# Optimization experiments

Measured on AMD Instinct MI355X. Metric: run time of the kernel, lower is better.

The kernel has to match this reference:

```python
import math
import jax, jax.numpy as jnp
import numpy as np

B, T, C, H = 4, 1024, 1024, 16


def setup_inputs() -> dict:
    key = jax.random.key(0)
    k1, k2, k3 = jax.random.split(key, 3)
    scale = 0.02
    return {
        "x": jax.random.normal(k1, (B, T, C), dtype=jnp.float32),
        "w_attn": jax.random.normal(k2, (C, 3 * C), dtype=jnp.float32) * scale,
        "b_attn": jnp.zeros((3 * C,), dtype=jnp.float32),
        "w_proj": jax.random.normal(k3, (C, C), dtype=jnp.float32) * scale,
        "b_proj": jnp.zeros((C,), dtype=jnp.float32),
    }


def reference(x, w_attn, b_attn, w_proj, b_proj):
    b, t, c = x.shape
    h = H
    d = c // h
    qkv = x @ w_attn + b_attn                      # [b, t, 3c]
    q, k, v = jnp.split(qkv, 3, axis=-1)
    # [b, h, t, d]
    q = q.reshape(b, t, h, d).transpose(0, 2, 1, 3)
    k = k.reshape(b, t, h, d).transpose(0, 2, 1, 3)
    v = v.reshape(b, t, h, d).transpose(0, 2, 1, 3)
    att = jnp.einsum("bhqd,bhkd->bhqk", q, k) * (1.0 / math.sqrt(d))
    causal = jnp.tril(jnp.ones((t, t), dtype=bool))
    att = jnp.where(causal[None, None], att, -jnp.inf)
    att = jax.nn.softmax(att, axis=-1)
    # dropout is identity in eval mode
    y = jnp.einsum("bhqk,bhkd->bhqd", att, v)      # [b, h, t, d]
    y = y.transpose(0, 2, 1, 3).reshape(b, t, c)
    return y @ w_proj + b_proj
```

## Files before the change

### kernel.cpp

```cpp
#include <hip/hip_runtime.h>

typedef __bf16 bf16;
typedef float f32x4 __attribute__((ext_vector_type(4)));
typedef bf16 bf16x4 __attribute__((ext_vector_type(4)));
typedef bf16 bf16x8 __attribute__((ext_vector_type(8)));

#define MFMA16(a, b, c) __builtin_amdgcn_mfma_f32_16x16x32_bf16((a), (b), (c), 0, 0, 0)

__device__ __forceinline__ f32x4 zero4() {
    f32x4 z; z[0] = 0.f; z[1] = 0.f; z[2] = 0.f; z[3] = 0.f; return z;
}
__device__ __forceinline__ void gl_lds16(const bf16* g, bf16* l) {
    __builtin_amdgcn_global_load_lds(
        (const __attribute__((address_space(1))) void*)g,
        (__attribute__((address_space(3))) void*)l, 16, 0, 0);
}

__global__ __launch_bounds__(256) void conv_k(const float* __restrict__ src,
                                              bf16* __restrict__ dst, int n)
{
    const int i = (blockIdx.x * 256 + threadIdx.x) * 8;
    if (i >= n) return;
    const float4 a = *(const float4*)(src + i);
    const float4 b = *(const float4*)(src + i + 4);
    bf16x8 o;
    o[0] = (bf16)a.x; o[1] = (bf16)a.y; o[2] = (bf16)a.z; o[3] = (bf16)a.w;
    o[4] = (bf16)b.x; o[5] = (bf16)b.y; o[6] = (bf16)b.z; o[7] = (bf16)b.w;
    *(bf16x8*)(dst + i) = o;
}

__global__ __launch_bounds__(256) void transp_k(const float* __restrict__ src,
                                                bf16* __restrict__ dst, int K, int N)
{
    __shared__ bf16 Ls[64][72];
    const int tid = threadIdx.x;
    const int k0 = blockIdx.y << 6;
    const int n0 = blockIdx.x << 6;
    #pragma unroll
    for (int it = 0; it < 4; ++it) {
        const int lin = (it << 10) + (tid << 2);
        const int r = lin >> 6, c = lin & 63;
        const float4 v = *(const float4*)(src + (size_t)(k0 + r) * N + n0 + c);
        bf16x4 o; o[0] = (bf16)v.x; o[1] = (bf16)v.y; o[2] = (bf16)v.z; o[3] = (bf16)v.w;
        *(bf16x4*)&Ls[r][c] = o;
    }
    __syncthreads();
    #pragma unroll
    for (int it = 0; it < 2; ++it) {
        const int lin = (it << 11) + (tid << 3);
        const int nn = lin >> 6, kk = lin & 63;
        bf16x8 o;
        #pragma unroll
        for (int j = 0; j < 8; ++j) o[j] = Ls[kk + j][nn];
        *(bf16x8*)(dst + (size_t)(n0 + nn) * K + k0 + kk) = o;
    }
}

template <int MODE, int BN>
__global__ __launch_bounds__(256)
void gemm_bt(const bf16* __restrict__ A, const bf16* __restrict__ Bt,
             const float* __restrict__ bias,
             bf16* __restrict__ qw, bf16* __restrict__ kw, bf16* __restrict__ vw,
             float* __restrict__ outf, int M, int N, int K)
{
    constexpr int BK = 32;
    constexpr int MF = (BN == 128) ? 4 : 2;
    constexpr int NF = 4;
    constexpr int AE = 128 * BK;
    constexpr int BE = BN * BK;

    __shared__ __align__(16) bf16 smem[2 * AE + 2 * BE];
    bf16* const As0 = smem;
    bf16* const As1 = smem + AE;
    bf16* const Bs0 = smem + 2 * AE;
    bf16* const Bs1 = smem + 2 * AE + BE;

    const int tid  = threadIdx.x;
    const int lane = tid & 63;
    const int wid  = tid >> 6;
    const int l16  = lane & 15;
    const int g    = lane >> 4;
    const int wrb  = (BN == 128) ? ((wid >> 1) << 6) : (wid << 5);
    const int wcb  = (BN == 128) ? ((wid & 1) << 6) : 0;
    const int m0   = blockIdx.y << 7;
    const int n0   = blockIdx.x * BN;

    const int srow = lane >> 2;
    const int schk = lane & 3;
    const int rA0 = (wid << 5) + srow;
    const int rA1 = rA0 + 16;
    const int rB0 = wid * (BN / 4) + srow;
    const int rB1 = rB0 + 16;
    const bf16* pa0 = A  + (size_t)(m0 + rA0) * K + ((schk ^ ((rA0 >> 1) & 3)) << 3);
    const bf16* pa1 = A  + (size_t)(m0 + rA1) * K + ((schk ^ ((rA1 >> 1) & 3)) << 3);
    const bf16* pb0 = Bt + (size_t)(n0 + rB0) * K + ((schk ^ ((rB0 >> 1) & 3)) << 3);
    const bf16* pb1 = Bt + (size_t)(n0 + rB1) * K + ((schk ^ ((rB1 >> 1) & 3)) << 3);
    const int dA0 = (wid << 5) * BK, dA1 = dA0 + 16 * BK;
    const int dB0 = (wid * (BN / 4)) * BK, dB1 = dB0 + 16 * BK;

    int offA[MF], offB[NF];
    #pragma unroll
    for (int mf = 0; mf < MF; ++mf) {
        const int r = wrb + (mf << 4) + l16;
        offA[mf] = r * BK + ((g ^ ((r >> 1) & 3)) << 3);
    }
    #pragma unroll
    for (int nf = 0; nf < NF; ++nf) {
        const int r = wcb + (nf << 4) + l16;
        offB[nf] = r * BK + ((g ^ ((r >> 1) & 3)) << 3);
    }

    f32x4 acc[MF][NF];
    #pragma unroll
    for (int i = 0; i < MF; ++i)
        #pragma unroll
        for (int j = 0; j < NF; ++j) acc[i][j] = zero4();

    const int nk = K >> 5;
    gl_lds16(pa0, As0 + dA0); gl_lds16(pa1, As0 + dA1);
    gl_lds16(pb0, Bs0 + dB0);
    if (BN == 128) gl_lds16(pb1, Bs0 + dB1);
    pa0 += BK; pa1 += BK; pb0 += BK; pb1 += BK;
    __syncthreads();

    for (int kt = 0; kt < nk; ++kt) {
        const bool odd = kt & 1;
        if (kt + 1 < nk) {
            bf16* an = odd ? As0 : As1;
            bf16* bn = odd ? Bs0 : Bs1;
            gl_lds16(pa0, an + dA0); gl_lds16(pa1, an + dA1);
            gl_lds16(pb0, bn + dB0);
            if (BN == 128) gl_lds16(pb1, bn + dB1);
            pa0 += BK; pa1 += BK; pb0 += BK; pb1 += BK;
        }
        const bf16* ac = odd ? As1 : As0;
        const bf16* bc = odd ? Bs1 : Bs0;
        bf16x8 af[MF], bfr[NF];
        #pragma unroll
        for (int mf = 0; mf < MF; ++mf) af[mf] = *(const bf16x8*)&ac[offA[mf]];
        #pragma unroll
        for (int nf = 0; nf < NF; ++nf) bfr[nf] = *(const bf16x8*)&bc[offB[nf]];
        #pragma unroll
        for (int mf = 0; mf < MF; ++mf)
            #pragma unroll
            for (int nf = 0; nf < NF; ++nf)
                acc[mf][nf] = MFMA16(af[mf], bfr[nf], acc[mf][nf]);
        __syncthreads();
    }

    if (MODE == 0) {
        bf16* const Es = smem;
        const int bq  = m0 >> 10;
        const int tb  = m0 & 1023;
        const int hh0 = (n0 & 1023) >> 6;
        const bool isV = (n0 >= 2048);
        if (isV) {
            #pragma unroll
            for (int mf = 0; mf < MF; ++mf)
                #pragma unroll
                for (int nf = 0; nf < NF; ++nf) {
                    const int nn = wcb + (nf << 4) + l16;
                    const float bs = bias[n0 + nn];
                    bf16x4 p;
                    #pragma unroll
                    for (int j = 0; j < 4; ++j) p[j] = (bf16)(acc[mf][nf][j] + bs);
                    const int m = wrb + (mf << 4) + (g << 2);
                    const int pp = ((m >> 5) << 5) + (((m >> 2) & 3) << 3) + (((m >> 4) & 1) << 2);
                    *(bf16x4*)&Es[nn * 128 + pp] = p;
                }
        } else {
            #pragma unroll
            for (int mf = 0; mf < MF; ++mf)
                #pragma unroll
                for (int nf = 0; nf < NF; ++nf) {
                    const int nn = wcb + (nf << 4) + l16;
                    const float bs = bias[n0 + nn];
                    #pragma unroll
                    for (int j = 0; j < 4; ++j) {
                        const int mm = wrb + (mf << 4) + (g << 2) + j;
                        Es[mm * 128 + nn] = (bf16)(acc[mf][nf][j] + bs);
                    }
                }
        }
        __syncthreads();
        #pragma unroll
        for (int it = 0; it < 8; ++it) {
            const int idx = (it << 8) + tid;
            const int row = idx >> 4, ch = idx & 15;
            const bf16x8 v = *(const bf16x8*)&Es[row * 128 + (ch << 3)];
            if (isV) {
                const int dd = row & 63, hh = hh0 + (row >> 6);
                *(bf16x8*)(vw + ((size_t)((bq << 4) + hh) << 16) + ((size_t)dd << 10)
                           + tb + (ch << 3)) = v;
            } else {
                const int t = tb + row;
                const int cc = ch << 3;
                const int hh = hh0 + (cc >> 6);
                bf16* const dst = (n0 < 1024) ? qw : kw;
                *(bf16x8*)(dst + ((size_t)((bq << 4) + hh) << 16) + ((size_t)t << 6)
                           + (cc & 63)) = v;
            }
        }
    } else {
        #pragma unroll
        for (int mf = 0; mf < MF; ++mf)
            #pragma unroll
            for (int nf = 0; nf < NF; ++nf) {
                const int ng = n0 + wcb + (nf << 4) + l16;
                const float bs = bias[ng];
                #pragma unroll
                for (int j = 0; j < 4; ++j) {
                    const int mg = m0 + wrb + (mf << 4) + (g << 2) + j;
                    outf[(size_t)mg * N + ng] = acc[mf][nf][j] + bs;
                }
            }
    }
}

__global__ __launch_bounds__(256)
void attn_k(const bf16* __restrict__ Qp, const bf16* __restrict__ Kp,
            const bf16* __restrict__ Vt, bf16* __restrict__ att)
{
    __shared__ __align__(16) bf16 Kl0[64 * 64], Kl1[64 * 64];
    __shared__ __align__(16) bf16 Vl0[64 * 64], Vl1[64 * 64];

    const int bx = blockIdx.x;
    const int bh = blockIdx.y;
    const int b  = bh >> 4, h = bh & 15;

    const int tid  = threadIdx.x;
    const int lane = tid & 63;
    const int wid  = tid >> 6;
    const int g    = lane >> 4;
    const int l16  = lane & 15;
    const int g8   = g << 3;

    const size_t hb = (size_t)bh << 16;
    const bf16* Qh = Qp + hb;
    const bf16* Kh = Kp + hb;
    const bf16* Vh = Vt + hb;

    const int srow = lane >> 3;
    const int sswz = ((lane & 7) ^ srow) << 3;
    const int kr0  = (wid << 4) + srow;
    const int kr1  = kr0 + 8;
    const int dst0 = (wid << 4) << 6;
    const int dst1 = ((wid << 4) + 8) << 6;

    int offKV[2][4];
    #pragma unroll
    for (int ks = 0; ks < 2; ++ks)
        #pragma unroll
        for (int cb = 0; cb < 4; ++cb) {
            const int r = (cb << 4) + l16;
            offKV[ks][cb] = (r << 6) + (((((ks << 2) + g)) ^ (r & 7)) << 3);
        }

    const float QSCALE = 0.125f * 1.44269504f;

    for (int pass = 0; pass < 2; ++pass) {
        const int qb = pass ? (15 - bx) : bx;
        const int q0 = qb << 6;

        const bf16* qp = Qh + ((size_t)(q0 + (wid << 4) + l16) << 6) + g8;
        bf16x8 qf0 = *(const bf16x8*)qp;
        bf16x8 qf1 = *(const bf16x8*)(qp + 32);
        #pragma unroll
        for (int e = 0; e < 8; ++e) {
            qf0[e] = (bf16)(QSCALE * (float)qf0[e]);
            qf1[e] = (bf16)(QSCALE * (float)qf1[e]);
        }

        f32x4 acc_o[4];
        float m_r = -1e30f, l_r = 0.f;
        #pragma unroll
        for (int i = 0; i < 4; ++i) acc_o[i] = zero4();

        gl_lds16(Kh + ((size_t)kr0 << 6) + sswz, Kl0 + dst0);
        gl_lds16(Kh + ((size_t)kr1 << 6) + sswz, Kl0 + dst1);
        gl_lds16(Vh + ((size_t)kr0 << 10) + sswz, Vl0 + dst0);
        gl_lds16(Vh + ((size_t)kr1 << 10) + sswz, Vl0 + dst1);
        __syncthreads();

        for (int kt = 0; kt <= qb; ++kt) {
            const bool odd = kt & 1;
            if (kt < qb) {
                const int kv1 = (kt + 1) << 6;
                bf16* Kn = odd ? Kl0 : Kl1;
                bf16* Vn = odd ? Vl0 : Vl1;
                gl_lds16(Kh + ((size_t)(kv1 + kr0) << 6) + sswz, Kn + dst0);
                gl_lds16(Kh + ((size_t)(kv1 + kr1) << 6) + sswz, Kn + dst1);
                gl_lds16(Vh + ((size_t)kr0 << 10) + kv1 + sswz, Vn + dst0);
                gl_lds16(Vh + ((size_t)kr1 << 10) + kv1 + sswz, Vn + dst1);
            }
            const bf16* Kc = odd ? Kl1 : Kl0;
            const bf16* Vc = odd ? Vl1 : Vl0;

            f32x4 sacc[4];
            #pragma unroll
            for (int cb = 0; cb < 4; ++cb) sacc[cb] = zero4();
            #pragma unroll
            for (int cb = 0; cb < 4; ++cb) {
                const bf16x8 kf = *(const bf16x8*)&Kc[offKV[0][cb]];
                sacc[cb] = MFMA16(kf, qf0, sacc[cb]);
            }
            #pragma unroll
            for (int cb = 0; cb < 4; ++cb) {
                const bf16x8 kf = *(const bf16x8*)&Kc[offKV[1][cb]];
                sacc[cb] = MFMA16(kf, qf1, sacc[cb]);
            }
            if (kt == qb) {
                const int qloc = (wid << 4) + l16;
                #pragma unroll
                for (int cb = 0; cb < 4; ++cb) {
                    #pragma unroll
                    for (int j = 0; j < 4; ++j) {
                        const int kvloc = (cb << 4) + (g << 2) + j;
                        if (kvloc > qloc) sacc[cb][j] = -1e30f;
                    }
                }
            }
            float pm = sacc[0][0];
            #pragma unroll
            for (int cb = 0; cb < 4; ++cb)
                #pragma unroll
                for (int j = 0; j < 4; ++j) pm = fmaxf(pm, sacc[cb][j]);
            pm = fmaxf(pm, __shfl_xor(pm, 16));
            pm = fmaxf(pm, __shfl_xor(pm, 32));
            if (__any(pm > m_r + 8.f)) {
                const float mn = fmaxf(m_r, pm);
                const float sc = __builtin_amdgcn_exp2f(m_r - mn);
                m_r = mn;
                l_r *= sc;
                #pragma unroll
                for (int db = 0; db < 4; ++db)
                    #pragma unroll
                    for (int j = 0; j < 4; ++j) acc_o[db][j] *= sc;
            }
            float rsum = 0.f;
            #pragma unroll
            for (int cb = 0; cb < 4; ++cb)
                #pragma unroll
                for (int j = 0; j < 4; ++j) {
                    const float p = __builtin_amdgcn_exp2f(sacc[cb][j] - m_r);
                    sacc[cb][j] = p;
                    rsum += p;
                }
            rsum += __shfl_xor(rsum, 16);
            rsum += __shfl_xor(rsum, 32);
            l_r += rsum;
            bf16x8 pf0, pf1;
            #pragma unroll
            for (int i = 0; i < 8; ++i) {
                pf0[i] = (bf16)sacc[i >> 2][i & 3];
                pf1[i] = (bf16)sacc[2 + (i >> 2)][i & 3];
            }
            #pragma unroll
            for (int db = 0; db < 4; ++db) {
                const bf16x8 vf = *(const bf16x8*)&Vc[offKV[0][db]];
                acc_o[db] = MFMA16(vf, pf0, acc_o[db]);
            }
            #pragma unroll
            for (int db = 0; db < 4; ++db) {
                const bf16x8 vf = *(const bf16x8*)&Vc[offKV[1][db]];
                acc_o[db] = MFMA16(vf, pf1, acc_o[db]);
            }
            __syncthreads();
        }

        const float inv_l = 1.f / l_r;
        const int t = q0 + (wid << 4) + l16;
        #pragma unroll
        for (int db = 0; db < 4; ++db) {
            bf16x4 o;
            #pragma unroll
            for (int j = 0; j < 4; ++j) o[j] = (bf16)(acc_o[db][j] * inv_l);
            *(bf16x4*)(att + (((size_t)b << 10) + t) * 1024 + (h << 6) + (db << 4) + (g << 2)) = o;
        }
        __syncthreads();
    }
}

extern "C" void kernel_launch(void* const* d_in, const int* in_sizes, int n_in,
                              void* d_out, int out_size, void* d_ws, size_t ws_size,
                              hipStream_t stream)
{
    const float* x      = (const float*)d_in[0];
    const float* w_attn = (const float*)d_in[1];
    const float* b_attn = (const float*)d_in[2];
    const float* w_proj = (const float*)d_in[3];
    const float* b_proj = (const float*)d_in[4];
    float* out = (float*)d_out;

    bf16* xb  = (bf16*)d_ws;
    bf16* wT  = xb  + (size_t)4096 * 1024;
    bf16* wpT = wT  + (size_t)3072 * 1024;
    bf16* qw  = wpT + (size_t)1024 * 1024;
    bf16* kw  = qw  + (size_t)64 * 1024 * 64;
    bf16* vw  = kw  + (size_t)64 * 1024 * 64;
    bf16* aw  = vw  + (size_t)64 * 1024 * 64;

    conv_k<<<2048, 256, 0, stream>>>(x, xb, 4096 * 1024);
    transp_k<<<dim3(48, 16), 256, 0, stream>>>(w_attn, wT, 1024, 3072);
    transp_k<<<dim3(16, 16), 256, 0, stream>>>(w_proj, wpT, 1024, 1024);

    gemm_bt<0, 128><<<dim3(24, 32), 256, 0, stream>>>(xb, wT, b_attn, qw, kw, vw,
                                                      nullptr, 4096, 3072, 1024);
    attn_k<<<dim3(8, 64), 256, 0, stream>>>(qw, kw, vw, aw);
    gemm_bt<1, 64><<<dim3(16, 32), 256, 0, stream>>>(aw, wpT, b_proj, nullptr, nullptr, nullptr,
                                                     out, 4096, 1024, 1024);
}
```

Measured before the change: 98.79 us.

## Triple-buffer GEMM K-loop with vmcnt waits and swap attention grid order

The GEMM main loop moves from double to triple LDS buffering. It prefetches two tiles ahead and replaces the trailing __syncthreads with an explicit s_waitcnt vmcnt plus s_barrier at the top of each iteration, and raises wave priority around the MFMA block. The goal is to hide global-to-LDS load latency and cut barrier stalls, at the cost of more shared memory per block, which may reduce occupancy. The attention launch grid is also transposed so that heads vary fastest across blocks, which changes the block scheduling order for causal work balance.

After: 94.01 us. 1.05x faster.

```diff
diff --git a/kernel.cpp b/kernel.cpp
--- a/kernel.cpp
+++ b/kernel.cpp
@@ -68,12 +68,11 @@
     constexpr int NF = 4;
     constexpr int AE = 128 * BK;
     constexpr int BE = BN * BK;
-
-    __shared__ __align__(16) bf16 smem[2 * AE + 2 * BE];
-    bf16* const As0 = smem;
-    bf16* const As1 = smem + AE;
-    bf16* const Bs0 = smem + 2 * AE;
-    bf16* const Bs1 = smem + 2 * AE + BE;
+    constexpr int LPI = (BN == 128) ? 4 : 3;
+
+    __shared__ __align__(16) bf16 smem[3 * (AE + BE)];
+    bf16* const Asb = smem;
+    bf16* const Bsb = smem + 3 * AE;
 
     const int tid  = threadIdx.x;
     const int lane = tid & 63;
@@ -98,6 +97,13 @@
     const int dA0 = (wid << 5) * BK, dA1 = dA0 + 16 * BK;
     const int dB0 = (wid * (BN / 4)) * BK, dB1 = dB0 + 16 * BK;
 
+    auto issue = [&](bf16* ab, bf16* bb) {
+        gl_lds16(pa0, ab + dA0); gl_lds16(pa1, ab + dA1);
+        gl_lds16(pb0, bb + dB0);
+        if constexpr (BN == 128) gl_lds16(pb1, bb + dB1);
+        pa0 += BK; pa1 += BK; pb0 += BK; pb1 += BK;
+    };
+
     int offA[MF], offB[NF];
     #pragma unroll
     for (int mf = 0; mf < MF; ++mf) {
@@ -117,36 +123,39 @@
         for (int j = 0; j < NF; ++j) acc[i][j] = zero4();
 
     const int nk = K >> 5;
-    gl_lds16(pa0, As0 + dA0); gl_lds16(pa1, As0 + dA1);
-    gl_lds16(pb0, Bs0 + dB0);
-    if (BN == 128) gl_lds16(pb1, Bs0 + dB1);
-    pa0 += BK; pa1 += BK; pb0 += BK; pb1 += BK;
-    __syncthreads();
+    issue(Asb, Bsb);
+    issue(Asb + AE, Bsb + BE);
 
     for (int kt = 0; kt < nk; ++kt) {
-        const bool odd = kt & 1;
-        if (kt + 1 < nk) {
-            bf16* an = odd ? As0 : As1;
-            bf16* bn = odd ? Bs0 : Bs1;
-            gl_lds16(pa0, an + dA0); gl_lds16(pa1, an + dA1);
-            gl_lds16(pb0, bn + dB0);
-            if (BN == 128) gl_lds16(pb1, bn + dB1);
-            pa0 += BK; pa1 += BK; pb0 += BK; pb1 += BK;
-        }
-        const bf16* ac = odd ? As1 : As0;
-        const bf16* bc = odd ? Bs1 : Bs0;
+        if (kt == nk - 1) {
+            asm volatile("s_waitcnt vmcnt(0)" ::: "memory");
+        } else {
+            if constexpr (LPI == 4) asm volatile("s_waitcnt vmcnt(4)" ::: "memory");
+            else                    asm volatile("s_waitcnt vmcnt(3)" ::: "memory");
+        }
+        __builtin_amdgcn_s_barrier();
+        const int nxt = kt + 2;
+        if (nxt < nk) {
+            const int s = nxt - (nxt / 3) * 3;
+            issue(Asb + s * AE, Bsb + s * BE);
+        }
+        const int c = kt - (kt / 3) * 3;
+        const bf16* ac = Asb + c * AE;
+        const bf16* bc = Bsb + c * BE;
         bf16x8 af[MF], bfr[NF];
         #pragma unroll
         for (int mf = 0; mf < MF; ++mf) af[mf] = *(const bf16x8*)&ac[offA[mf]];
         #pragma unroll
         for (int nf = 0; nf < NF; ++nf) bfr[nf] = *(const bf16x8*)&bc[offB[nf]];
+        __builtin_amdgcn_s_setprio(1);
         #pragma unroll
         for (int mf = 0; mf < MF; ++mf)
             #pragma unroll
             for (int nf = 0; nf < NF; ++nf)
                 acc[mf][nf] = MFMA16(af[mf], bfr[nf], acc[mf][nf]);
-        __syncthreads();
-    }
+        __builtin_amdgcn_s_setprio(0);
+    }
+    __syncthreads();
 
     if (MODE == 0) {
         bf16* const Es = smem;
@@ -224,8 +233,8 @@
     __shared__ __align__(16) bf16 Kl0[64 * 64], Kl1[64 * 64];
     __shared__ __align__(16) bf16 Vl0[64 * 64], Vl1[64 * 64];
 
-    const int bx = blockIdx.x;
-    const int bh = blockIdx.y;
+    const int bh = blockIdx.x;
+    const int bx = blockIdx.y;
     const int b  = bh >> 4, h = bh & 15;
 
     const int tid  = threadIdx.x;
@@ -406,7 +415,7 @@
 
     gemm_bt<0, 128><<<dim3(24, 32), 256, 0, stream>>>(xb, wT, b_attn, qw, kw, vw,
                                                       nullptr, 4096, 3072, 1024);
-    attn_k<<<dim3(8, 64), 256, 0, stream>>>(qw, kw, vw, aw);
+    attn_k<<<dim3(64, 8), 256, 0, stream>>>(qw, kw, vw, aw);
     gemm_bt<1, 64><<<dim3(16, 32), 256, 0, stream>>>(aw, wpT, b_proj, nullptr, nullptr, nullptr,
                                                      out, 4096, 1024, 1024);
 }
```
